# Kernel tuning notes

Measured on AMD Instinct MI355X. Metric: run time of the kernel, lower is better.

The kernel has to match this reference:

```python
import jax, jax.numpy as jnp
import numpy as np

N, E, T = 4096, 49152, 262144
H, EMB, AIN, EB, TB = 256, 64, 92, 80, 40
NBLK = 12  # 4 alignn * 2 EGGC + 4 gcn


def _ln(x, s, b):
    mu = jnp.mean(x, -1, keepdims=True)
    v = jnp.mean((x - mu) ** 2, -1, keepdims=True)
    return (x - mu) * jax.lax.rsqrt(v + 1e-5) * s + b


def _mlp(x, W, b, s, bi):
    # Linear -> LayerNorm -> SiLU (MLPLayer)
    return jax.nn.silu(_ln(x @ W + b, s, bi))


def _rbf(x, vmin, vmax, bins):
    centers = jnp.linspace(vmin, vmax, bins)
    gamma = 1.0 / ((vmax - vmin) / (bins - 1))
    return jnp.exp(-gamma * (x[:, None] - centers) ** 2)


def _eggc(x, e, src, dst, W, b, ln_s, ln_b, n_nodes):
    # W: [5,H,H] = src_gate, dst_gate, edge_gate, src_update, dst_update
    m = (x @ W[0] + b[0])[src] + (x @ W[1] + b[1])[dst] + (e @ W[2] + b[2])
    sigma = jax.nn.sigmoid(m)
    sum_sh = jax.ops.segment_sum((x @ W[4] + b[4])[src] * sigma, dst, num_segments=n_nodes)
    sum_s = jax.ops.segment_sum(sigma, dst, num_segments=n_nodes)
    h = sum_sh / (sum_s + 1e-6)
    x_new = jax.nn.silu(_ln(x @ W[3] + b[3] + h, ln_s[0], ln_b[0]))
    e_new = jax.nn.silu(_ln(m, ln_s[1], ln_b[1]))
    return x + x_new, e + e_new  # residual=True


def setup_inputs() -> dict:
    key = jax.random.key(0)
    ks = jax.random.split(key, 16)
    s = 0.05
    return {
        "atom_features": jax.random.normal(ks[0], (N, AIN), jnp.float32),
        "r": jax.random.normal(ks[1], (E, 3), jnp.float32),
        "src": jax.random.randint(ks[2], (E,), 0, N),
        "dst": jax.random.randint(ks[3], (E,), 0, N),
        "lsrc": jax.random.randint(ks[4], (T,), 0, E),
        "ldst": jax.random.randint(ks[5], (T,), 0, E),
        "atom_W": s * jax.random.normal(ks[6], (AIN, H), jnp.float32),
        "atom_b": jnp.zeros((H,), jnp.float32),
        "atom_ln_s": jnp.ones((H,), jnp.float32),
        "atom_ln_b": jnp.zeros((H,), jnp.float32),
        "edge_W1": s * jax.random.normal(ks[7], (EB, EMB), jnp.float32),
        "edge_b1": jnp.zeros((EMB,), jnp.float32),
        "edge_ln1_s": jnp.ones((EMB,), jnp.float32),
        "edge_ln1_b": jnp.zeros((EMB,), jnp.float32),
        "edge_W2": s * jax.random.normal(ks[8], (EMB, H), jnp.float32),
        "edge_b2": jnp.zeros((H,), jnp.float32),
        "edge_ln2_s": jnp.ones((H,), jnp.float32),
        "edge_ln2_b": jnp.zeros((H,), jnp.float32),
        "ang_W1": s * jax.random.normal(ks[9], (TB, EMB), jnp.float32),
        "ang_b1": jnp.zeros((EMB,), jnp.float32),
        "ang_ln1_s": jnp.ones((EMB,), jnp.float32),
        "ang_ln1_b": jnp.zeros((EMB,), jnp.float32),
        "ang_W2": s * jax.random.normal(ks[10], (EMB, H), jnp.float32),
        "ang_b2": jnp.zeros((H,), jnp.float32),
        "ang_ln2_s": jnp.ones((H,), jnp.float32),
        "ang_ln2_b": jnp.zeros((H,), jnp.float32),
        "eggc_W": s * jax.random.normal(ks[11], (NBLK, 5, H, H), jnp.float32),
        "eggc_b": jnp.zeros((NBLK, 5, H), jnp.float32),
        "eggc_ln_s": jnp.ones((NBLK, 2, H), jnp.float32),
        "eggc_ln_b": jnp.zeros((NBLK, 2, H), jnp.float32),
        "fc_W": s * jax.random.normal(ks[12], (H, 1), jnp.float32),
        "fc_b": jnp.zeros((1,), jnp.float32),
    }


def reference(atom_features, r, src, dst, lsrc, ldst,
              atom_W, atom_b, atom_ln_s, atom_ln_b,
              edge_W1, edge_b1, edge_ln1_s, edge_ln1_b,
              edge_W2, edge_b2, edge_ln2_s, edge_ln2_b,
              ang_W1, ang_b1, ang_ln1_s, ang_ln1_b,
              ang_W2, ang_b2, ang_ln2_s, ang_ln2_b,
              eggc_W, eggc_b, eggc_ln_s, eggc_ln_b, fc_W, fc_b):
    # line-graph bond cosines: cos(-r_i, r_j) for each bond pair
    r1, r2 = -r[lsrc], r[ldst]
    cos = jnp.sum(r1 * r2, -1) / (jnp.linalg.norm(r1, axis=-1) * jnp.linalg.norm(r2, axis=-1))
    cos = jnp.clip(cos, -1.0, 1.0)
    z = _mlp(_mlp(_rbf(cos, -1.0, 1.0, TB), ang_W1, ang_b1, ang_ln1_s, ang_ln1_b),
             ang_W2, ang_b2, ang_ln2_s, ang_ln2_b)
    x = _mlp(atom_features, atom_W, atom_b, atom_ln_s, atom_ln_b)
    bondlength = jnp.linalg.norm(r, axis=1)
    y = _mlp(_mlp(_rbf(bondlength, 0.0, 8.0, EB), edge_W1, edge_b1, edge_ln1_s, edge_ln1_b),
             edge_W2, edge_b2, edge_ln2_s, edge_ln2_b)
    for i in range(4):  # alignn layers: crystal graph then line graph
        x, m = _eggc(x, y, src, dst, eggc_W[2 * i], eggc_b[2 * i], eggc_ln_s[2 * i], eggc_ln_b[2 * i], N)
        y, z = _eggc(m, z, lsrc, ldst, eggc_W[2 * i + 1], eggc_b[2 * i + 1], eggc_ln_s[2 * i + 1], eggc_ln_b[2 * i + 1], E)
    for i in range(4):  # gcn layers
        j = 8 + i
        x, y = _eggc(x, y, src, dst, eggc_W[j], eggc_b[j], eggc_ln_s[j], eggc_ln_b[j], N)
    atomwise_energy = x @ fc_W + fc_b  # [N,1]
    total_energy = jnp.mean(atomwise_energy)  # AvgPooling (eV/atom), single graph
    return total_energy, atomwise_energy
```

## Files before the change

### kernel.cpp

```cpp
#include <hip/hip_runtime.h>


typedef unsigned short bfu;
typedef __attribute__((ext_vector_type(8))) short short8;
typedef __attribute__((ext_vector_type(4))) float floatx4;

#define CHN 4096
#define CHCAP 24576
#define HH 65536

__device__ __forceinline__ float bf2f(bfu u) {
  union { unsigned u; float f; } x; x.u = ((unsigned)u) << 16; return x.f;
}
__device__ __forceinline__ bfu f2bf(float f) {
  union { float f; unsigned u; } x; x.f = f;
  unsigned r = x.u + 0x7FFFu + ((x.u >> 16) & 1u);
  return (bfu)(r >> 16);
}
__device__ __forceinline__ float fsig(float x) {
  return __builtin_amdgcn_rcpf(1.f + __expf(-x));
}
__device__ __forceinline__ float fsilu(float x) { return x * fsig(x); }

struct f4 { float x, y, z, w; };
__device__ __forceinline__ f4 ld4(const bfu* p) {
  ushort4 u = *(const ushort4*)(const void*)p;
  return {bf2f(u.x), bf2f(u.y), bf2f(u.z), bf2f(u.w)};
}
__device__ __forceinline__ void st4(bfu* p, f4 v) {
  ushort4 u = {f2bf(v.x), f2bf(v.y), f2bf(v.z), f2bf(v.w)};
  *(ushort4*)(void*)p = u;
}
__device__ __forceinline__ f4 f4add(f4 a, f4 b) { return {a.x+b.x, a.y+b.y, a.z+b.z, a.w+b.w}; }
__device__ __forceinline__ f4 sig4(f4 m) {
  return {fsig(m.x), fsig(m.y), fsig(m.z), fsig(m.w)};
}
__device__ __forceinline__ void wstats(f4 v, float& mean, float& rstd) {
  float s = v.x+v.y+v.z+v.w;
  float q = v.x*v.x+v.y*v.y+v.z*v.z+v.w*v.w;
#pragma unroll
  for (int m = 1; m < 64; m <<= 1) { s += __shfl_xor(s, m); q += __shfl_xor(q, m); }
  mean = s * (1.f/256.f);
  rstd = rsqrtf(fmaxf(q*(1.f/256.f) - mean*mean, 0.f) + 1e-5f);
}
__device__ __forceinline__ f4 lnsilu4(f4 pre, f4 sg, f4 bb) {
  float mean, rstd; wstats(pre, mean, rstd);
  f4 u = {(pre.x-mean)*rstd*sg.x+bb.x, (pre.y-mean)*rstd*sg.y+bb.y,
          (pre.z-mean)*rstd*sg.z+bb.z, (pre.w-mean)*rstd*sg.w+bb.w};
  return {fsilu(u.x), fsilu(u.y), fsilu(u.z), fsilu(u.w)};
}
__device__ __forceinline__ float block_sum256(float t, float* sm) {
#pragma unroll
  for (int o = 32; o; o >>= 1) t += __shfl_down(t, o);
  if ((threadIdx.x & 63) == 0) sm[threadIdx.x >> 6] = t;
  __syncthreads();
  float r = sm[0] + sm[1] + sm[2] + sm[3];
  __syncthreads();
  return r;
}

__global__ void probe_kernel(const unsigned* __restrict__ ones_raw, int* __restrict__ mode) {
  if (threadIdx.x == 0) *mode = (ones_raw[0] == 0x3F800000u) ? 1 : 0;
}
__global__ __launch_bounds__(256) void cvt_kernel(
    const void* __restrict__ src, bfu* __restrict__ dst, int n, const int* __restrict__ mode) {
  int i = blockIdx.x * 256 + threadIdx.x;
  if (i >= n) return;
  dst[i] = (*mode) ? f2bf(((const float*)src)[i]) : ((const bfu*)src)[i];
}
__global__ __launch_bounds__(256) void cvtf_kernel(
    const void* __restrict__ src, float* __restrict__ dst, int n, const int* __restrict__ mode) {
  int i = blockIdx.x * 256 + threadIdx.x;
  if (i >= n) return;
  dst[i] = (*mode) ? ((const float*)src)[i] : bf2f(((const bfu*)src)[i]);
}
struct CvtDesc { const void* src; bfu* dst; int n; };
struct CvtPack { CvtDesc e[20]; };
__global__ __launch_bounds__(256) void cvt_batch_kernel(CvtPack p, const int* __restrict__ mode) {
  CvtDesc d = p.e[blockIdx.y];
  int i = blockIdx.x * 256 + threadIdx.x;
  if (i >= d.n) return;
  d.dst[i] = (*mode) ? f2bf(((const float*)d.src)[i]) : ((const bfu*)d.src)[i];
}

template<int BM, int BN, int WR, int WC>
__device__ __forceinline__ void gemm_body(
    const bfu* __restrict__ A, const bfu* __restrict__ Bt,
    const bfu* __restrict__ bias, bfu* __restrict__ Cout,
    int cnt, int N, int K, int base, int m0, int n0)
{
  constexpr int WM = BM / WR, WN = BN / WC;
  constexpr int TM = WM / 16, TN = WN / 16;
  constexpr int LDT = 72;
  static __shared__ bfu As[BM * LDT];
  static __shared__ bfu Bs[BN * LDT];

  const int tid = threadIdx.x, wave = tid >> 6, lane = tid & 63;
  const int wr = wave / WC, wc = wave % WC;
  const int lrow = lane & 15, kq = (lane >> 4) * 8;

  floatx4 acc[TM][TN];
#pragma unroll
  for (int i = 0; i < TM; ++i)
#pragma unroll
    for (int j = 0; j < TN; ++j) acc[i][j] = (floatx4){0.f, 0.f, 0.f, 0.f};

  constexpr int ACH = BM * 8, BCH = BN * 8;
  for (int k0 = 0; k0 < K; k0 += 64) {
#pragma unroll
    for (int idx = tid; idx < ACH; idx += 256) {
      int row = idx >> 3, kc = (idx & 7) << 3;
      int r = m0 + row;
      int ar = base + (r < cnt ? r : cnt - 1);
      *(short8*)(void*)(As + row * LDT + kc) =
          *(const short8*)(const void*)(A + (size_t)ar * K + k0 + kc);
    }
#pragma unroll
    for (int idx = tid; idx < BCH; idx += 256) {
      int row = idx >> 3, kc = (idx & 7) << 3;
      *(short8*)(void*)(Bs + row * LDT + kc) =
          *(const short8*)(const void*)(Bt + (size_t)(n0 + row) * K + k0 + kc);
    }
    __syncthreads();
#pragma unroll
    for (int s = 0; s < 2; ++s) {
      short8 Af[TM], Bf[TN];
#pragma unroll
      for (int i = 0; i < TM; ++i)
        Af[i] = *(const short8*)(const void*)(As + (wr * WM + i * 16 + lrow) * LDT + s * 32 + kq);
#pragma unroll
      for (int j = 0; j < TN; ++j)
        Bf[j] = *(const short8*)(const void*)(Bs + (wc * WN + j * 16 + lrow) * LDT + s * 32 + kq);
#pragma unroll
      for (int i = 0; i < TM; ++i)
#pragma unroll
        for (int j = 0; j < TN; ++j)
          acc[i][j] = __builtin_amdgcn_mfma_f32_16x16x32_bf16(Af[i], Bf[j], acc[i][j], 0, 0, 0);
    }
    __syncthreads();
  }

  const int rquad = lane >> 4, cin = lane & 15;
#pragma unroll
  for (int i = 0; i < TM; ++i) {
#pragma unroll
    for (int rr = 0; rr < 4; ++rr) {
      int orow = m0 + wr * WM + i * 16 + rquad * 4 + rr;
      if (orow >= cnt) continue;
#pragma unroll
      for (int j = 0; j < TN; ++j) {
        int gcol = n0 + wc * WN + j * 16 + cin;
        Cout[(size_t)orow * N + gcol] = f2bf(acc[i][j][rr] + bf2f(bias[gcol]));
      }
    }
  }
}

template<int BM, int BN, int WR, int WC>
__global__ __launch_bounds__(256) void gemm_kernel(
    const bfu* __restrict__ A, const bfu* __restrict__ Bt,
    const bfu* __restrict__ bias, bfu* __restrict__ Cout, int M, int N, int K)
{
  gemm_body<BM, BN, WR, WC>(A, Bt, bias, Cout, M, N, K, 0,
                            blockIdx.x * BM, blockIdx.y * BN);
}

__global__ __launch_bounds__(256) void line_gemm_kernel(
    const bfu* __restrict__ z, const bfu* __restrict__ yb,
    const bfu* __restrict__ W, const bfu* __restrict__ bb,
    bfu* __restrict__ mchunk, bfu* __restrict__ u3c,
    const int* __restrict__ loff, int n0, int n1)
{
  if (blockIdx.y < 2) {
    int base = loff[n0], cnt = loff[n1] - base;
    int m0 = blockIdx.x * 128;
    if (m0 >= cnt) return;
    gemm_body<128, 128, 2, 2>(z, W + 4 * HH, bb + 4 * 256, mchunk,
                              cnt, 256, 256, base, m0, blockIdx.y * 128);
  } else {
    if (blockIdx.x >= 64) return;
    gemm_body<128, 128, 2, 2>(yb + (size_t)n0 * 256, W + 3 * HH, bb + 3 * 256, u3c,
                              CHN, 256, 256, 0, (blockIdx.x & 31) * 128, (blockIdx.x >> 5) * 128);
  }
}

__global__ __launch_bounds__(256) void cosbl_kernel(
    const float* __restrict__ r, const int* __restrict__ lsrc_p,
    const int* __restrict__ ldst_p, float* __restrict__ cosv,
    float* __restrict__ bl, int T, int E)
{
  int idx = blockIdx.x * 256 + threadIdx.x;
  if (idx < T) {
    int e1 = lsrc_p[idx], e2 = ldst_p[idx];
    float ax = -r[e1 * 3 + 0], ay = -r[e1 * 3 + 1], az = -r[e1 * 3 + 2];
    float bx =  r[e2 * 3 + 0], by =  r[e2 * 3 + 1], bz =  r[e2 * 3 + 2];
    float dot = ax * bx + ay * by + az * bz;
    float na = sqrtf(ax * ax + ay * ay + az * az);
    float nb = sqrtf(bx * bx + by * by + bz * bz);
    float c = dot / (na * nb);
    cosv[idx] = fminf(1.f, fmaxf(-1.f, c));
  } else if (idx < T + E) {
    int e = idx - T;
    float x = r[e * 3 + 0], yv = r[e * 3 + 1], zv = r[e * 3 + 2];
    bl[e] = sqrtf(x * x + yv * yv + zv * zv);
  }
}

template<int KP, int BINS, int IS_ANG>
__global__ __launch_bounds__(256) void mlp1_ln_kernel(
    const float* __restrict__ v, const bfu* __restrict__ Bt,
    const bfu* __restrict__ bias, const bfu* __restrict__ lns,
    const bfu* __restrict__ lnb, bfu* __restrict__ outp, int M)
{
  constexpr int LDT = KP + 8;
  __shared__ bfu As[128 * LDT];
  __shared__ bfu Bs[64 * LDT];
  const int tid = threadIdx.x, wave = tid >> 6, lane = tid & 63;
  const int lrow = lane & 15, kq = (lane >> 4) * 8;
  const int m0 = blockIdx.x * 128;

  for (int idx = tid; idx < 128 * (KP / 8); idx += 256) {
    int row = idx / (KP / 8), kc = (idx % (KP / 8)) * 8;
    float val = v[m0 + row];
    short8 pack;
#pragma unroll
    for (int jj = 0; jj < 8; ++jj) {
      int k = kc + jj;
      float e = 0.f;
      if (k < BINS) {
        float center = IS_ANG ? (-1.f + k * (2.f / 39.f)) : (k * (8.f / 79.f));
        float d = val - center;
        e = __expf((IS_ANG ? -19.5f : -9.875f) * d * d);
      }
      ((bfu*)&pack)[jj] = f2bf(e);
    }
    *(short8*)(void*)(As + row * LDT + kc) = pack;
  }
  for (int idx = tid; idx < 64 * (KP / 8); idx += 256) {
    int row = idx / (KP / 8), kc = (idx % (KP / 8)) * 8;
    *(short8*)(void*)(Bs + row * LDT + kc) =
        *(const short8*)(const void*)(Bt + (size_t)row * KP + kc);
  }
  __syncthreads();

  floatx4 acc[2][4];
#pragma unroll
  for (int i = 0; i < 2; ++i)
#pragma unroll
    for (int j = 0; j < 4; ++j) acc[i][j] = (floatx4){0.f, 0.f, 0.f, 0.f};
#pragma unroll
  for (int ks = 0; ks < KP / 32; ++ks) {
    short8 Af[2], Bf[4];
#pragma unroll
    for (int i = 0; i < 2; ++i)
      Af[i] = *(const short8*)(const void*)(As + (wave * 32 + i * 16 + lrow) * LDT + ks * 32 + kq);
#pragma unroll
    for (int j = 0; j < 4; ++j)
      Bf[j] = *(const short8*)(const void*)(Bs + (j * 16 + lrow) * LDT + ks * 32 + kq);
#pragma unroll
    for (int i = 0; i < 2; ++i)
#pragma unroll
      for (int j = 0; j < 4; ++j)
        acc[i][j] = __builtin_amdgcn_mfma_f32_16x16x32_bf16(Af[i], Bf[j], acc[i][j], 0, 0, 0);
  }

  const int rquad = lane >> 4, cin = lane & 15;
  float bj[4], sj[4], lj[4];
#pragma unroll
  for (int j = 0; j < 4; ++j) {
    bj[j] = bf2f(bias[j * 16 + cin]);
    sj[j] = bf2f(lns[j * 16 + cin]);
    lj[j] = bf2f(lnb[j * 16 + cin]);
  }
#pragma unroll
  for (int i = 0; i < 2; ++i) {
#pragma unroll
    for (int rr = 0; rr < 4; ++rr) {
      int row = m0 + wave * 32 + i * 16 + rquad * 4 + rr;
      float pre[4], s = 0.f, q = 0.f;
#pragma unroll
      for (int j = 0; j < 4; ++j) {
        pre[j] = acc[i][j][rr] + bj[j];
        s += pre[j]; q += pre[j] * pre[j];
      }
#pragma unroll
      for (int mm = 1; mm < 16; mm <<= 1) { s += __shfl_xor(s, mm); q += __shfl_xor(q, mm); }
      float mean = s * (1.f / 64.f);
      float rstd = rsqrtf(fmaxf(q * (1.f / 64.f) - mean * mean, 0.f) + 1e-5f);
#pragma unroll
      for (int j = 0; j < 4; ++j) {
        float u = (pre[j] - mean) * rstd * sj[j] + lj[j];
        outp[(size_t)row * 64 + j * 16 + cin] = f2bf(fsilu(u));
      }
    }
  }
}

__global__ __launch_bounds__(256) void mlp2_ln_kernel(
    const bfu* __restrict__ A, const bfu* __restrict__ Bt,
    const bfu* __restrict__ bias, const bfu* __restrict__ lns,
    const bfu* __restrict__ lnb, bfu* __restrict__ outp, int M)
{
  __shared__ bfu As[64 * 72];
  __shared__ bfu Bs[256 * 72];
  __shared__ float part[64 * 8];
  const int tid = threadIdx.x, wave = tid >> 6, lane = tid & 63;
  const int lrow = lane & 15, kq = (lane >> 4) * 8;
  const int m0 = blockIdx.x * 64;

  for (int idx = tid; idx < 512; idx += 256) {
    int row = idx >> 3, kc = (idx & 7) << 3;
    *(short8*)(void*)(As + row * 72 + kc) =
        *(const short8*)(const void*)(A + (size_t)(m0 + row) * 64 + kc);
  }
  for (int idx = tid; idx < 2048; idx += 256) {
    int row = idx >> 3, kc = (idx & 7) << 3;
    *(short8*)(void*)(Bs + row * 72 + kc) =
        *(const short8*)(const void*)(Bt + (size_t)row * 64 + kc);
  }
  __syncthreads();

  floatx4 acc[4][4];
#pragma unroll
  for (int i = 0; i < 4; ++i)
#pragma unroll
    for (int j = 0; j < 4; ++j) acc[i][j] = (floatx4){0.f, 0.f, 0.f, 0.f};
#pragma unroll
  for (int s = 0; s < 2; ++s) {
    short8 Af[4], Bf[4];
#pragma unroll
    for (int i = 0; i < 4; ++i)
      Af[i] = *(const short8*)(const void*)(As + (i * 16 + lrow) * 72 + s * 32 + kq);
#pragma unroll
    for (int j = 0; j < 4; ++j)
      Bf[j] = *(const short8*)(const void*)(Bs + (wave * 64 + j * 16 + lrow) * 72 + s * 32 + kq);
#pragma unroll
    for (int i = 0; i < 4; ++i)
#pragma unroll
      for (int j = 0; j < 4; ++j)
        acc[i][j] = __builtin_amdgcn_mfma_f32_16x16x32_bf16(Af[i], Bf[j], acc[i][j], 0, 0, 0);
  }

  const int rquad = lane >> 4, cin = lane & 15;
  float bj[4], sj[4], lj[4];
#pragma unroll
  for (int j = 0; j < 4; ++j) {
    int col = wave * 64 + j * 16 + cin;
    bj[j] = bf2f(bias[col]); sj[j] = bf2f(lns[col]); lj[j] = bf2f(lnb[col]);
  }
#pragma unroll
  for (int i = 0; i < 4; ++i) {
#pragma unroll
    for (int rr = 0; rr < 4; ++rr) {
      float s = 0.f, q = 0.f;
#pragma unroll
      for (int j = 0; j < 4; ++j) {
        float p = acc[i][j][rr] + bj[j];
        s += p; q += p * p;
      }
#pragma unroll
      for (int mm = 1; mm < 16; mm <<= 1) { s += __shfl_xor(s, mm); q += __shfl_xor(q, mm); }
      if (cin == 0) {
        int row = i * 16 + rquad * 4 + rr;
        part[row * 8 + wave * 2] = s;
        part[row * 8 + wave * 2 + 1] = q;
      }
    }
  }
  __syncthreads();
#pragma unroll
  for (int i = 0; i < 4; ++i) {
#pragma unroll
    for (int rr = 0; rr < 4; ++rr) {
      int row = i * 16 + rquad * 4 + rr;
      float s = part[row * 8] + part[row * 8 + 2] + part[row * 8 + 4] + part[row * 8 + 6];
      float q = part[row * 8 + 1] + part[row * 8 + 3] + part[row * 8 + 5] + part[row * 8 + 7];
      float mean = s * (1.f / 256.f);
      float rstd = rsqrtf(fmaxf(q * (1.f / 256.f) - mean * mean, 0.f) + 1e-5f);
#pragma unroll
      for (int j = 0; j < 4; ++j) {
        float u = (acc[i][j][rr] + bj[j] - mean) * rstd * sj[j] + lj[j];
        outp[(size_t)(m0 + row) * 256 + wave * 64 + j * 16 + cin] = f2bf(fsilu(u));
      }
    }
  }
}

__global__ __launch_bounds__(256) void count_kernel(
    const int* __restrict__ d, int* __restrict__ cnt, int ne) {
  int i = blockIdx.x * 256 + threadIdx.x;
  if (i < ne) atomicAdd(&cnt[d[i]], 1);
}
__global__ __launch_bounds__(256) void scan_kernel(
    const int* __restrict__ cnt, int* __restrict__ off, int n) {
  __shared__ int ssum[256];
  __shared__ int sbase[257];
  int t = threadIdx.x;
  int strip = (n + 255) / 256;
  int lo = t * strip, hi = lo + strip; if (hi > n) hi = n; if (lo > n) lo = n;
  int s = 0;
  for (int i = lo; i < hi; ++i) s += cnt[i];
  ssum[t] = s;
  __syncthreads();
  if (t == 0) {
    int run = 0;
    for (int i = 0; i < 256; ++i) { sbase[i] = run; run += ssum[i]; }
    sbase[256] = run;
  }
  __syncthreads();
  int run = sbase[t];
  for (int i = lo; i < hi; ++i) { off[i] = run; run += cnt[i]; }
  if (t == 0) off[n] = sbase[256];
}
__global__ __launch_bounds__(256) void copy_kernel(
    const int* __restrict__ a, int* __restrict__ b, int n) {
  int i = blockIdx.x * 256 + threadIdx.x;
  if (i < n) b[i] = a[i];
}
__global__ __launch_bounds__(256) void fill_kernel(
    const int* __restrict__ d, int* __restrict__ cur, int* __restrict__ ids, int ne) {
  int i = blockIdx.x * 256 + threadIdx.x;
  if (i < ne) ids[atomicAdd(&cur[d[i]], 1)] = i;
}
__global__ __launch_bounds__(256) void fill2_kernel(
    const int* __restrict__ ldst, const int* __restrict__ lsrc, int* __restrict__ cur,
    int* __restrict__ lsrc_p, int* __restrict__ ldst_p, int ne) {
  int i = blockIdx.x * 256 + threadIdx.x;
  if (i >= ne) return;
  int d = ldst[i];
  int pos = atomicAdd(&cur[d], 1);
  lsrc_p[pos] = lsrc[i];
  ldst_p[pos] = d;
}

__global__ __launch_bounds__(256) void transpose_pad_kernel(
    const void* __restrict__ W, bfu* __restrict__ Wt, int K, int N, int Kp,
    const int* __restrict__ mode)
{
  int idx = blockIdx.x * 256 + threadIdx.x;
  if (idx >= N * Kp) return;
  int n = idx / Kp, k = idx - n * Kp;
  bfu v = 0;
  if (k < K) {
    size_t si = (size_t)k * N + n;
    v = (*mode) ? f2bf(((const float*)W)[si]) : ((const bfu*)W)[si];
  }
  Wt[idx] = v;
}
__device__ __forceinline__ int slot2mat(int slot) {
  const int m[5] = {0, 4, 1, 3, 2};
  return m[slot];
}
__global__ __launch_bounds__(256) void transpose_eggc_kernel(
    const void* __restrict__ W, bfu* __restrict__ Wt, const int* __restrict__ mode)
{
  int bs = blockIdx.y;
  int blk = bs / 5, slot = bs - blk * 5;
  int mat = slot2mat(slot);
  int idx = blockIdx.x * 256 + threadIdx.x;
  int n = idx >> 8, k = idx & 255;
  size_t si = ((size_t)(blk * 5 + mat) * 256 + k) * 256 + n;
  bfu v = (*mode) ? f2bf(((const float*)W)[si]) : ((const bfu*)W)[si];
  Wt[((size_t)bs * 256 + n) * 256 + k] = v;
}
__global__ __launch_bounds__(256) void bias_perm_kernel(
    const void* __restrict__ B, bfu* __restrict__ Bp, const int* __restrict__ mode)
{
  int i = blockIdx.x * 256 + threadIdx.x;
  int bs = i >> 8, c = i & 255;
  int blk = bs / 5, slot = bs - blk * 5;
  int mat = slot2mat(slot);
  size_t si = (size_t)(blk * 5 + mat) * 256 + c;
  Bp[i] = (*mode) ? f2bf(((const float*)B)[si]) : ((const bfu*)B)[si];
}

__global__ __launch_bounds__(256) void atom_fused_kernel(
    const bfu* __restrict__ mbuf, const bfu* __restrict__ af,
    const int* __restrict__ src, const int* __restrict__ dst,
    bfu* __restrict__ X, bfu* __restrict__ Y,
    const int* __restrict__ aoff, const int* __restrict__ aids,
    int eblk,
    const bfu* __restrict__ lns, const bfu* __restrict__ lnb,
    const bfu* __restrict__ les, const bfu* __restrict__ leb)
{
  int wave = threadIdx.x >> 6, c4 = (threadIdx.x & 63) * 4;
  if ((int)blockIdx.x < eblk) {
    int e = blockIdx.x * 4 + wave;
    f4 m = f4add(f4add(ld4(mbuf + (size_t)e * 256 + c4),
                       ld4(af + (size_t)src[e] * 1024 + c4)),
                 ld4(af + (size_t)dst[e] * 1024 + 512 + c4));
    f4 sil = lnsilu4(m, ld4(les + c4), ld4(leb + c4));
    bfu* op = Y + (size_t)e * 256 + c4;
    st4(op, f4add(sil, ld4(op)));
  } else {
    int n = (blockIdx.x - eblk) * 4 + wave;
    int p0 = aoff[n], p1 = aoff[n + 1];
    f4 g1 = ld4(af + (size_t)n * 1024 + 512 + c4);
    f4 num = {0, 0, 0, 0}, den = {0, 0, 0, 0};
    for (int p = p0; p < p1; ++p) {
      int id = aids[p], sx = src[id];
      f4 m = f4add(f4add(ld4(mbuf + (size_t)id * 256 + c4),
                         ld4(af + (size_t)sx * 1024 + c4)), g1);
      f4 sg = sig4(m);
      f4 u4 = ld4(af + (size_t)sx * 1024 + 256 + c4);
      num.x += sg.x * u4.x; num.y += sg.y * u4.y; num.z += sg.z * u4.z; num.w += sg.w * u4.w;
      den = f4add(den, sg);
    }
    f4 u3 = ld4(af + (size_t)n * 1024 + 768 + c4);
    f4 pre = {u3.x + num.x / (den.x + 1e-6f), u3.y + num.y / (den.y + 1e-6f),
              u3.z + num.z / (den.z + 1e-6f), u3.w + num.w / (den.w + 1e-6f)};
    f4 sil = lnsilu4(pre, ld4(lns + c4), ld4(lnb + c4));
    bfu* op = X + (size_t)n * 256 + c4;
    st4(op, f4add(sil, ld4(op)));
  }
}

__global__ __launch_bounds__(256) void line_fused_kernel(
    const bfu* __restrict__ mchunk, const bfu* __restrict__ lf,
    const bfu* __restrict__ u3c,
    const int* __restrict__ loff, const int* __restrict__ lsrc_p,
    const int* __restrict__ ldst_p,
    bfu* __restrict__ Z, bfu* __restrict__ Y,
    int n0, int eblk,
    const bfu* __restrict__ lns, const bfu* __restrict__ lnb,
    const bfu* __restrict__ les, const bfu* __restrict__ leb)
{
  int wave = threadIdx.x >> 6, c4 = (threadIdx.x & 63) * 4;
  int base = loff[n0];
  if ((int)blockIdx.x < eblk) {
    int rloc = blockIdx.x * 4 + wave;
    int cnt = loff[n0 + CHN] - base;
    if (rloc >= cnt) return;
    int p = base + rloc;
    f4 m = f4add(f4add(ld4(mchunk + (size_t)rloc * 256 + c4),
                       ld4(lf + (size_t)lsrc_p[p] * 768 + c4)),
                 ld4(lf + (size_t)ldst_p[p] * 768 + 512 + c4));
    f4 sil = lnsilu4(m, ld4(les + c4), ld4(leb + c4));
    bfu* op = Z + (size_t)p * 256 + c4;
    st4(op, f4add(sil, ld4(op)));
  } else {
    int n = n0 + (blockIdx.x - eblk) * 4 + wave;
    int p0 = loff[n], p1 = loff[n + 1];
    f4 g1 = ld4(lf + (size_t)n * 768 + 512 + c4);
    f4 num = {0, 0, 0, 0}, den = {0, 0, 0, 0};
    for (int p = p0; p < p1; ++p) {
      int sx = lsrc_p[p];
      f4 m = f4add(f4add(ld4(mchunk + (size_t)(p - base) * 256 + c4),
                         ld4(lf + (size_t)sx * 768 + c4)), g1);
      f4 sg = sig4(m);
      f4 u4 = ld4(lf + (size_t)sx * 768 + 256 + c4);
      num.x += sg.x * u4.x; num.y += sg.y * u4.y; num.z += sg.z * u4.z; num.w += sg.w * u4.w;
      den = f4add(den, sg);
    }
    f4 u3 = ld4(u3c + (size_t)(n - n0) * 256 + c4);
    f4 pre = {u3.x + num.x / (den.x + 1e-6f), u3.y + num.y / (den.y + 1e-6f),
              u3.z + num.z / (den.z + 1e-6f), u3.w + num.w / (den.w + 1e-6f)};
    f4 sil = lnsilu4(pre, ld4(lns + c4), ld4(lnb + c4));
    bfu* op = Y + (size_t)n * 256 + c4;
    st4(op, f4add(sil, ld4(op)));
  }
}

__global__ __launch_bounds__(256) void atom_init_kernel(
    const bfu* __restrict__ af, const bfu* __restrict__ W, const bfu* __restrict__ bias,
    const bfu* __restrict__ lns, const bfu* __restrict__ lnb, bfu* __restrict__ X)
{
  __shared__ float sm[4];
  int row = blockIdx.x, c = threadIdx.x;
  float acc = bf2f(bias[c]);
  for (int k = 0; k < 92; ++k)
    acc += bf2f(af[row * 92 + k]) * bf2f(W[k * 256 + c]);
  float mean = block_sum256(acc, sm) * (1.f / 256.f);
  float d = acc - mean;
  float var = block_sum256(d * d, sm) * (1.f / 256.f);
  float u = d * rsqrtf(var + 1e-5f) * bf2f(lns[c]) + bf2f(lnb[c]);
  X[(size_t)row * 256 + c] = f2bf(fsilu(u));
}

__global__ __launch_bounds__(256) void final_kernel(
    const bfu* __restrict__ X, const bfu* __restrict__ fcW, const bfu* __restrict__ fcb,
    void* __restrict__ out, float* __restrict__ acc, const int* __restrict__ mode)
{
  int row = blockIdx.x * 4 + (threadIdx.x >> 6);
  int lane = threadIdx.x & 63;
  float s = 0.f;
#pragma unroll
  for (int k = 0; k < 4; ++k)
    s += bf2f(X[(size_t)row * 256 + lane + k * 64]) * bf2f(fcW[lane + k * 64]);
#pragma unroll
  for (int o = 32; o; o >>= 1) s += __shfl_down(s, o);
  if (lane == 0) {
    float v = s + bf2f(fcb[0]);
    if (*mode) ((float*)out)[1 + row] = v;
    else       ((bfu*)out)[1 + row] = f2bf(v);
    atomicAdd(acc, v);
  }
}
__global__ void mean_kernel(const float* __restrict__ acc, void* __restrict__ out,
                            const int* __restrict__ mode) {
  if (threadIdx.x == 0) {
    float v = acc[0] * (1.f / 4096.f);
    if (*mode) ((float*)out)[0] = v;
    else       ((bfu*)out)[0] = f2bf(v);
  }
}
__global__ void dbg_kernel(void* __restrict__ out, float v) {
  if (threadIdx.x == 0) { ((bfu*)out)[0] = f2bf(v); }
}

static void gemm128(const bfu* A, const bfu* Bt, const bfu* bias, bfu* C,
                    int M, int N, int K, hipStream_t st) {
  if (N % 128 == 0) {
    dim3 g(M / 128, N / 128);
    gemm_kernel<128, 128, 2, 2><<<g, 256, 0, st>>>(A, Bt, bias, C, M, N, K);
  } else {
    dim3 g(M / 128, N / 64);
    gemm_kernel<128, 64, 4, 1><<<g, 256, 0, st>>>(A, Bt, bias, C, M, N, K);
  }
}

extern "C" void kernel_launch(void* const* d_in, const int* in_sizes, int n_in,
                              void* d_out, int out_size, void* d_ws, size_t ws_size,
                              hipStream_t stream) {
  const int N = 4096, E = 49152, T = 262144, H = 256;

  const int* src  = (const int*)d_in[2];
  const int* dst  = (const int*)d_in[3];
  const int* lsrc = (const int*)d_in[4];
  const int* ldst = (const int*)d_in[5];

  char* bp = (char*)d_ws;
  size_t off = 0;
  auto carve = [&](size_t bytes) -> char* {
    char* q = bp + off;
    off = (off + bytes + 255) & ~(size_t)255;
    return q;
  };
  bfu* x       = (bfu*)carve((size_t)N * H * 2);
  bfu* y       = (bfu*)carve((size_t)E * H * 2);
  bfu* z       = (bfu*)carve((size_t)T * H * 2);
  bfu* reg     = (bfu*)carve((size_t)E * 768 * 2);
  bfu* u3c     = (bfu*)carve((size_t)CHN * H * 2);
  bfu* mchunk  = (bfu*)carve((size_t)CHCAP * H * 2);
  bfu* WtE     = (bfu*)carve((size_t)60 * H * H * 2);
  bfu* ebp     = (bfu*)carve((size_t)12 * 5 * H * 2);
  bfu* Wt_a1   = (bfu*)carve(64 * 64 * 2);
  bfu* Wt_a2   = (bfu*)carve(256 * 64 * 2);
  bfu* Wt_e1   = (bfu*)carve(64 * 128 * 2);
  bfu* Wt_e2   = (bfu*)carve(256 * 64 * 2);
  int* aoff    = (int*)carve((size_t)(N + 1) * 4);
  int* aids    = (int*)carve((size_t)E * 4);
  int* loff    = (int*)carve((size_t)(E + 1) * 4);
  int* lsrc_p  = (int*)carve((size_t)T * 4);
  int* ldst_p  = (int*)carve((size_t)T * 4);
  int* cursors = (int*)carve((size_t)E * 4);
  float* macc  = (float*)carve(256);
  int* mode    = (int*)carve(256);
  bfu* par_c   = (bfu*)carve(8192 * 2);
  bfu* els_c   = (bfu*)carve((size_t)12 * 2 * H * 2);
  bfu* elb_c   = (bfu*)carve((size_t)12 * 2 * H * 2);

  if (off > ws_size) {
    hipMemsetAsync(d_out, 0, (size_t)out_size * 2, stream);
    dbg_kernel<<<1, 64, 0, stream>>>(d_out, (float)(ws_size >> 20));
    return;
  }

  char* tail = (char*)reg + (size_t)52 * 1024 * 1024;
  bfu* af_c  = (bfu*)tail;                 tail += ((size_t)N * 92 * 2 + 255) & ~255ull;
  float* r_f = (float*)tail;               tail += ((size_t)E * 3 * 4 + 255) & ~255ull;
  float* cosv = (float*)tail;              tail += ((size_t)T * 4 + 255) & ~255ull;
  float* blv = (float*)tail;               tail += ((size_t)E * 4 + 255) & ~255ull;
  bfu* atW_c = (bfu*)tail;

  bfu* atom_b_c   = par_c + 0;
  bfu* atom_lns_c = par_c + 256;
  bfu* atom_lnb_c = par_c + 512;
  bfu* e_b1_c     = par_c + 768;
  bfu* e_l1s_c    = par_c + 832;
  bfu* e_l1b_c    = par_c + 896;
  bfu* e_b2_c     = par_c + 1024;
  bfu* e_l2s_c    = par_c + 1280;
  bfu* e_l2b_c    = par_c + 1536;
  bfu* a_b1_c     = par_c + 1792;
  bfu* a_l1s_c    = par_c + 1856;
  bfu* a_l1b_c    = par_c + 1920;
  bfu* a_b2_c     = par_c + 2048;
  bfu* a_l2s_c    = par_c + 2304;
  bfu* a_l2b_c    = par_c + 2560;
  bfu* fcW_c      = par_c + 2816;
  bfu* fcb_c      = par_c + 3072;

  bfu* lfused = reg;
  bfu* afused = reg;
  bfu* mbufa  = reg + (size_t)N * 1024;
  bfu* emb_t  = reg;
  bfu* emb_e  = reg + (size_t)T * 64;

  probe_kernel<<<1, 64, 0, stream>>>((const unsigned*)d_in[8], mode);
  CvtPack pk;
  int ii = 0;
  auto add = [&](int idx, bfu* dstp, int n) { pk.e[ii++] = {d_in[idx], dstp, n}; };
  add(7, atom_b_c, 256);  add(8, atom_lns_c, 256); add(9, atom_lnb_c, 256);
  add(11, e_b1_c, 64);    add(12, e_l1s_c, 64);    add(13, e_l1b_c, 64);
  add(15, e_b2_c, 256);   add(16, e_l2s_c, 256);   add(17, e_l2b_c, 256);
  add(19, a_b1_c, 64);    add(20, a_l1s_c, 64);    add(21, a_l1b_c, 64);
  add(23, a_b2_c, 256);   add(24, a_l2s_c, 256);   add(25, a_l2b_c, 256);
  add(30, fcW_c, 256);    add(31, fcb_c, 1);
  add(28, els_c, 12 * 2 * 256);
  add(29, elb_c, 12 * 2 * 256);
  add(6, atW_c, 92 * 256);
  cvt_batch_kernel<<<dim3(92, 20), 256, 0, stream>>>(pk, mode);
  cvt_kernel<<<(N * 92 + 255) / 256, 256, 0, stream>>>(d_in[0], af_c, N * 92, mode);
  cvtf_kernel<<<(E * 3 + 255) / 256, 256, 0, stream>>>(d_in[1], r_f, E * 3, mode);

  hipMemsetAsync(cursors, 0, (size_t)N * 4, stream);
  count_kernel<<<E / 256, 256, 0, stream>>>(dst, cursors, E);
  scan_kernel<<<1, 256, 0, stream>>>(cursors, aoff, N);
  copy_kernel<<<(N + 255) / 256, 256, 0, stream>>>(aoff, cursors, N);
  fill_kernel<<<E / 256, 256, 0, stream>>>(dst, cursors, aids, E);

  hipMemsetAsync(cursors, 0, (size_t)E * 4, stream);
  count_kernel<<<T / 256, 256, 0, stream>>>(ldst, cursors, T);
  scan_kernel<<<1, 256, 0, stream>>>(cursors, loff, E);
  copy_kernel<<<(E + 255) / 256, 256, 0, stream>>>(loff, cursors, E);
  fill2_kernel<<<T / 256, 256, 0, stream>>>(ldst, lsrc, cursors, lsrc_p, ldst_p, T);

  transpose_eggc_kernel<<<dim3(256, 60), 256, 0, stream>>>(d_in[26], WtE, mode);
  bias_perm_kernel<<<60, 256, 0, stream>>>(d_in[27], ebp, mode);
  transpose_pad_kernel<<<16, 256, 0, stream>>>(d_in[18], Wt_a1, 40, 64, 64, mode);
  transpose_pad_kernel<<<64, 256, 0, stream>>>(d_in[22], Wt_a2, 64, 256, 64, mode);
  transpose_pad_kernel<<<32, 256, 0, stream>>>(d_in[10], Wt_e1, 80, 64, 128, mode);
  transpose_pad_kernel<<<64, 256, 0, stream>>>(d_in[14], Wt_e2, 64, 256, 64, mode);

  cosbl_kernel<<<(T + E + 255) / 256, 256, 0, stream>>>(r_f, lsrc_p, ldst_p, cosv, blv, T, E);
  mlp1_ln_kernel<64, 40, 1><<<T / 128, 256, 0, stream>>>(
      cosv, Wt_a1, a_b1_c, a_l1s_c, a_l1b_c, emb_t, T);
  mlp2_ln_kernel<<<T / 64, 256, 0, stream>>>(emb_t, Wt_a2, a_b2_c, a_l2s_c, a_l2b_c, z, T);
  mlp1_ln_kernel<128, 80, 0><<<E / 128, 256, 0, stream>>>(
      blv, Wt_e1, e_b1_c, e_l1s_c, e_l1b_c, emb_e, E);
  mlp2_ln_kernel<<<E / 64, 256, 0, stream>>>(emb_e, Wt_e2, e_b2_c, e_l2s_c, e_l2b_c, y, E);

  atom_init_kernel<<<N, 256, 0, stream>>>(af_c, atW_c, atom_b_c, atom_lns_c, atom_lnb_c, x);

  auto atom_eggc = [&](int blk, int do_edge) {
    const bfu* W  = WtE + (size_t)blk * 5 * HH;
    const bfu* bb = ebp + (size_t)blk * 5 * H;
    const bfu* ls = els_c + (size_t)blk * 2 * H;
    const bfu* lb = elb_c + (size_t)blk * 2 * H;
    gemm128(x, W, bb, afused, N, 1024, H, stream);
    gemm128(y, W + 4 * HH, bb + 4 * H, mbufa, E, H, H, stream);
    int eblk = do_edge ? E / 4 : 0;
    atom_fused_kernel<<<eblk + N / 4, 256, 0, stream>>>(
        mbufa, afused, src, dst, x, y, aoff, aids, eblk, ls, lb, ls + H, lb + H);
  };

  auto line_eggc = [&](int blk, int do_edge) {
    const bfu* W  = WtE + (size_t)blk * 5 * HH;
    const bfu* bb = ebp + (size_t)blk * 5 * H;
    const bfu* ls = els_c + (size_t)blk * 2 * H;
    const bfu* lb = elb_c + (size_t)blk * 2 * H;
    gemm128(y, W, bb, lfused, E, 768, H, stream);
    for (int c = 0; c < E / CHN; ++c) {
      int n0 = c * CHN;
      line_gemm_kernel<<<dim3(CHCAP / 128, 3), 256, 0, stream>>>(
          z, y, W, bb, mchunk, u3c, loff, n0, n0 + CHN);
      int eblk = do_edge ? CHCAP / 4 : 0;
      line_fused_kernel<<<eblk + CHN / 4, 256, 0, stream>>>(
          mchunk, lfused, u3c, loff, lsrc_p, ldst_p, z, y, n0, eblk,
          ls, lb, ls + H, lb + H);
    }
  };

  for (int i = 0; i < 4; ++i) {
    atom_eggc(2 * i, 1);
    line_eggc(2 * i + 1, i < 3);
  }
  for (int i = 0; i < 4; ++i)
    atom_eggc(8 + i, i < 3);

  hipMemsetAsync(macc, 0, 4, stream);
  final_kernel<<<N / 4, 256, 0, stream>>>(x, fcW_c, fcb_c, d_out, macc, mode);
  mean_kernel<<<1, 64, 0, stream>>>(macc, d_out, mode);
}
```

Before: 3.012 ms.

## Merge EGGC gemm launches, widen fused kernels to 8-wide, load MLP weights directly

The two atom-side GEMMs become one launch, and the line-graph gate GEMM is merged with the first chunk's edge/u3 GEMMs. The fused edge and node kernels now use 8-element vector loads with half-wave rows, so each wave handles two edges, or splits a node's neighbour loop across two halves and combines them with a shuffle. The MLP kernels read weight fragments straight from global memory instead of staging them in LDS. The goal is fewer launches, wider memory transactions and more memory-level parallelism in the gathers. The risks are lower occupancy from extra registers and uncoalesced global weight reads.

```diff
diff --git a/kernel.cpp b/kernel.cpp
--- a/kernel.cpp
+++ b/kernel.cpp
@@ -22,33 +22,50 @@
 }
 __device__ __forceinline__ float fsilu(float x) { return x * fsig(x); }
 
-struct f4 { float x, y, z, w; };
-__device__ __forceinline__ f4 ld4(const bfu* p) {
-  ushort4 u = *(const ushort4*)(const void*)p;
-  return {bf2f(u.x), bf2f(u.y), bf2f(u.z), bf2f(u.w)};
-}
-__device__ __forceinline__ void st4(bfu* p, f4 v) {
-  ushort4 u = {f2bf(v.x), f2bf(v.y), f2bf(v.z), f2bf(v.w)};
-  *(ushort4*)(void*)p = u;
-}
-__device__ __forceinline__ f4 f4add(f4 a, f4 b) { return {a.x+b.x, a.y+b.y, a.z+b.z, a.w+b.w}; }
-__device__ __forceinline__ f4 sig4(f4 m) {
-  return {fsig(m.x), fsig(m.y), fsig(m.z), fsig(m.w)};
-}
-__device__ __forceinline__ void wstats(f4 v, float& mean, float& rstd) {
-  float s = v.x+v.y+v.z+v.w;
-  float q = v.x*v.x+v.y*v.y+v.z*v.z+v.w*v.w;
-#pragma unroll
-  for (int m = 1; m < 64; m <<= 1) { s += __shfl_xor(s, m); q += __shfl_xor(q, m); }
-  mean = s * (1.f/256.f);
-  rstd = rsqrtf(fmaxf(q*(1.f/256.f) - mean*mean, 0.f) + 1e-5f);
-}
-__device__ __forceinline__ f4 lnsilu4(f4 pre, f4 sg, f4 bb) {
-  float mean, rstd; wstats(pre, mean, rstd);
-  f4 u = {(pre.x-mean)*rstd*sg.x+bb.x, (pre.y-mean)*rstd*sg.y+bb.y,
-          (pre.z-mean)*rstd*sg.z+bb.z, (pre.w-mean)*rstd*sg.w+bb.w};
-  return {fsilu(u.x), fsilu(u.y), fsilu(u.z), fsilu(u.w)};
-}
+struct f8 { float v[8]; };
+__device__ __forceinline__ f8 ld8(const bfu* p) {
+  short8 u = *(const short8*)(const void*)p;
+  f8 r;
+#pragma unroll
+  for (int i = 0; i < 8; ++i) r.v[i] = bf2f((bfu)u[i]);
+  return r;
+}
+__device__ __forceinline__ void st8(bfu* p, f8 x) {
+  short8 u;
+#pragma unroll
+  for (int i = 0; i < 8; ++i) u[i] = (short)f2bf(x.v[i]);
+  *(short8*)(void*)p = u;
+}
+__device__ __forceinline__ f8 add8(f8 a, f8 b) {
+  f8 r;
+#pragma unroll
+  for (int i = 0; i < 8; ++i) r.v[i] = a.v[i] + b.v[i];
+  return r;
+}
+__device__ __forceinline__ f8 sig8(f8 m) {
+  f8 r;
+#pragma unroll
+  for (int i = 0; i < 8; ++i) r.v[i] = fsig(m.v[i]);
+  return r;
+}
+__device__ __forceinline__ void wstats32(const f8& x, float& mean, float& rstd) {
+  float s = 0.f, q = 0.f;
+#pragma unroll
+  for (int i = 0; i < 8; ++i) { s += x.v[i]; q += x.v[i] * x.v[i]; }
+#pragma unroll
+  for (int m = 1; m < 32; m <<= 1) { s += __shfl_xor(s, m); q += __shfl_xor(q, m); }
+  mean = s * (1.f / 256.f);
+  rstd = rsqrtf(fmaxf(q * (1.f / 256.f) - mean * mean, 0.f) + 1e-5f);
+}
+__device__ __forceinline__ f8 lnsilu8(f8 pre, f8 sg, f8 bb) {
+  float mean, rstd; wstats32(pre, mean, rstd);
+  f8 r;
+#pragma unroll
+  for (int i = 0; i < 8; ++i)
+    r.v[i] = fsilu((pre.v[i] - mean) * rstd * sg.v[i] + bb.v[i]);
+  return r;
+}
+
 __device__ __forceinline__ float block_sum256(float t, float* sm) {
 #pragma unroll
   for (int o = 32; o; o >>= 1) t += __shfl_down(t, o);
@@ -180,6 +197,43 @@
   } else {
     if (blockIdx.x >= 64) return;
     gemm_body<128, 128, 2, 2>(yb + (size_t)n0 * 256, W + 3 * HH, bb + 3 * 256, u3c,
+                              CHN, 256, 256, 0, (blockIdx.x & 31) * 128, (blockIdx.x >> 5) * 128);
+  }
+}
+
+__global__ __launch_bounds__(256) void atom_gemm_kernel(
+    const bfu* __restrict__ x, const bfu* __restrict__ y,
+    const bfu* __restrict__ W, const bfu* __restrict__ bb,
+    bfu* __restrict__ afused, bfu* __restrict__ mbufa)
+{
+  if (blockIdx.x < 384) {
+    gemm_body<128, 128, 2, 2>(y, W + 4 * HH, bb + 4 * 256, mbufa,
+                              49152, 256, 256, 0, blockIdx.x * 128, blockIdx.y * 128);
+  } else {
+    int lid = (blockIdx.x - 384) * 2 + blockIdx.y;
+    gemm_body<128, 128, 2, 2>(x, W, bb, afused,
+                              4096, 1024, 256, 0, (lid >> 3) * 128, (lid & 7) * 128);
+  }
+}
+
+__global__ __launch_bounds__(256) void line_gates_kernel(
+    const bfu* __restrict__ y, const bfu* __restrict__ z,
+    const bfu* __restrict__ W, const bfu* __restrict__ bb,
+    bfu* __restrict__ lfused, bfu* __restrict__ mchunk, bfu* __restrict__ u3c,
+    const int* __restrict__ loff)
+{
+  if (blockIdx.y < 6) {
+    gemm_body<128, 128, 2, 2>(y, W, bb, lfused,
+                              49152, 768, 256, 0, blockIdx.x * 128, blockIdx.y * 128);
+  } else if (blockIdx.y < 8) {
+    int cnt = loff[CHN];
+    int m0 = blockIdx.x * 128;
+    if (blockIdx.x >= CHCAP / 128 || m0 >= cnt) return;
+    gemm_body<128, 128, 2, 2>(z, W + 4 * HH, bb + 4 * 256, mchunk,
+                              cnt, 256, 256, 0, m0, (blockIdx.y - 6) * 128);
+  } else {
+    if (blockIdx.x >= 64) return;
+    gemm_body<128, 128, 2, 2>(y, W + 3 * HH, bb + 3 * 256, u3c,
                               CHN, 256, 256, 0, (blockIdx.x & 31) * 128, (blockIdx.x >> 5) * 128);
   }
 }
@@ -214,7 +268,6 @@
 {
   constexpr int LDT = KP + 8;
   __shared__ bfu As[128 * LDT];
-  __shared__ bfu Bs[64 * LDT];
   const int tid = threadIdx.x, wave = tid >> 6, lane = tid & 63;
   const int lrow = lane & 15, kq = (lane >> 4) * 8;
   const int m0 = blockIdx.x * 128;
@@ -232,14 +285,9 @@
         float d = val - center;
         e = __expf((IS_ANG ? -19.5f : -9.875f) * d * d);
       }
-      ((bfu*)&pack)[jj] = f2bf(e);
+      pack[jj] = (short)f2bf(e);
     }
     *(short8*)(void*)(As + row * LDT + kc) = pack;
-  }
-  for (int idx = tid; idx < 64 * (KP / 8); idx += 256) {
-    int row = idx / (KP / 8), kc = (idx % (KP / 8)) * 8;
-    *(short8*)(void*)(Bs + row * LDT + kc) =
-        *(const short8*)(const void*)(Bt + (size_t)row * KP + kc);
   }
   __syncthreads();
 
@@ -252,11 +300,11 @@
   for (int ks = 0; ks < KP / 32; ++ks) {
     short8 Af[2], Bf[4];
 #pragma unroll
+    for (int j = 0; j < 4; ++j)
+      Bf[j] = *(const short8*)(const void*)(Bt + (size_t)(j * 16 + lrow) * KP + ks * 32 + kq);
+#pragma unroll
     for (int i = 0; i < 2; ++i)
       Af[i] = *(const short8*)(const void*)(As + (wave * 32 + i * 16 + lrow) * LDT + ks * 32 + kq);
-#pragma unroll
-    for (int j = 0; j < 4; ++j)
-      Bf[j] = *(const short8*)(const void*)(Bs + (j * 16 + lrow) * LDT + ks * 32 + kq);
 #pragma unroll
     for (int i = 0; i < 2; ++i)
 #pragma unroll
@@ -302,22 +350,24 @@
     const bfu* __restrict__ lnb, bfu* __restrict__ outp, int M)
 {
   __shared__ bfu As[64 * 72];
-  __shared__ bfu Bs[256 * 72];
   __shared__ float part[64 * 8];
   const int tid = threadIdx.x, wave = tid >> 6, lane = tid & 63;
   const int lrow = lane & 15, kq = (lane >> 4) * 8;
   const int m0 = blockIdx.x * 64;
 
+  short8 Bf[2][4];
+#pragma unroll
+  for (int s = 0; s < 2; ++s)
+#pragma unroll
+    for (int j = 0; j < 4; ++j)
+      Bf[s][j] = *(const short8*)(const void*)(
+          Bt + (size_t)(wave * 64 + j * 16 + lrow) * 64 + s * 32 + kq);
+
   for (int idx = tid; idx < 512; idx += 256) {
     int row = idx >> 3, kc = (idx & 7) << 3;
     *(short8*)(void*)(As + row * 72 + kc) =
         *(const short8*)(const void*)(A + (size_t)(m0 + row) * 64 + kc);
   }
-  for (int idx = tid; idx < 2048; idx += 256) {
-    int row = idx >> 3, kc = (idx & 7) << 3;
-    *(short8*)(void*)(Bs + row * 72 + kc) =
-        *(const short8*)(const void*)(Bt + (size_t)row * 64 + kc);
-  }
   __syncthreads();
 
   floatx4 acc[4][4];
@@ -327,18 +377,15 @@
     for (int j = 0; j < 4; ++j) acc[i][j] = (floatx4){0.f, 0.f, 0.f, 0.f};
 #pragma unroll
   for (int s = 0; s < 2; ++s) {
-    short8 Af[4], Bf[4];
+    short8 Af[4];
 #pragma unroll
     for (int i = 0; i < 4; ++i)
       Af[i] = *(const short8*)(const void*)(As + (i * 16 + lrow) * 72 + s * 32 + kq);
 #pragma unroll
-    for (int j = 0; j < 4; ++j)
-      Bf[j] = *(const short8*)(const void*)(Bs + (wave * 64 + j * 16 + lrow) * 72 + s * 32 + kq);
-#pragma unroll
     for (int i = 0; i < 4; ++i)
 #pragma unroll
       for (int j = 0; j < 4; ++j)
-        acc[i][j] = __builtin_amdgcn_mfma_f32_16x16x32_bf16(Af[i], Bf[j], acc[i][j], 0, 0, 0);
+        acc[i][j] = __builtin_amdgcn_mfma_f32_16x16x32_bf16(Af[i], Bf[s][j], acc[i][j], 0, 0, 0);
   }
 
   const int rquad = lane >> 4, cin = lane & 15;
@@ -483,35 +530,48 @@
     const bfu* __restrict__ lns, const bfu* __restrict__ lnb,
     const bfu* __restrict__ les, const bfu* __restrict__ leb)
 {
-  int wave = threadIdx.x >> 6, c4 = (threadIdx.x & 63) * 4;
+  int wave = threadIdx.x >> 6, lane = threadIdx.x & 63;
+  int half = lane >> 5, c8 = (lane & 31) * 8;
   if ((int)blockIdx.x < eblk) {
-    int e = blockIdx.x * 4 + wave;
-    f4 m = f4add(f4add(ld4(mbuf + (size_t)e * 256 + c4),
-                       ld4(af + (size_t)src[e] * 1024 + c4)),
-                 ld4(af + (size_t)dst[e] * 1024 + 512 + c4));
-    f4 sil = lnsilu4(m, ld4(les + c4), ld4(leb + c4));
-    bfu* op = Y + (size_t)e * 256 + c4;
-    st4(op, f4add(sil, ld4(op)));
+    int e = blockIdx.x * 8 + wave * 2 + half;
+    f8 m = add8(add8(ld8(mbuf + (size_t)e * 256 + c8),
+                     ld8(af + (size_t)src[e] * 1024 + c8)),
+                ld8(af + (size_t)dst[e] * 1024 + 512 + c8));
+    f8 sil = lnsilu8(m, ld8(les + c8), ld8(leb + c8));
+    bfu* op = Y + (size_t)e * 256 + c8;
+    st8(op, add8(sil, ld8(op)));
   } else {
     int n = (blockIdx.x - eblk) * 4 + wave;
     int p0 = aoff[n], p1 = aoff[n + 1];
-    f4 g1 = ld4(af + (size_t)n * 1024 + 512 + c4);
-    f4 num = {0, 0, 0, 0}, den = {0, 0, 0, 0};
-    for (int p = p0; p < p1; ++p) {
+    f8 g1 = ld8(af + (size_t)n * 1024 + 512 + c8);
+    f8 num = {}, den = {};
+    for (int p = p0 + half; p < p1; p += 2) {
       int id = aids[p], sx = src[id];
-      f4 m = f4add(f4add(ld4(mbuf + (size_t)id * 256 + c4),
-                         ld4(af + (size_t)sx * 1024 + c4)), g1);
-      f4 sg = sig4(m);
-      f4 u4 = ld4(af + (size_t)sx * 1024 + 256 + c4);
-      num.x += sg.x * u4.x; num.y += sg.y * u4.y; num.z += sg.z * u4.z; num.w += sg.w * u4.w;
-      den = f4add(den, sg);
-    }
-    f4 u3 = ld4(af + (size_t)n * 1024 + 768 + c4);
-    f4 pre = {u3.x + num.x / (den.x + 1e-6f), u3.y + num.y / (den.y + 1e-6f),
-              u3.z + num.z / (den.z + 1e-6f), u3.w + num.w / (den.w + 1e-6f)};
-    f4 sil = lnsilu4(pre, ld4(lns + c4), ld4(lnb + c4));
-    bfu* op = X + (size_t)n * 256 + c4;
-    st4(op, f4add(sil, ld4(op)));
+      f8 m = add8(add8(ld8(mbuf + (size_t)id * 256 + c8),
+                       ld8(af + (size_t)sx * 1024 + c8)), g1);
+      f8 sg = sig8(m);
+      f8 u4 = ld8(af + (size_t)sx * 1024 + 256 + c8);
+#pragma unroll
+      for (int i = 0; i < 8; ++i) {
+        num.v[i] += sg.v[i] * u4.v[i];
+        den.v[i] += sg.v[i];
+      }
+    }
+#pragma unroll
+    for (int i = 0; i < 8; ++i) {
+      num.v[i] += __shfl_xor(num.v[i], 32);
+      den.v[i] += __shfl_xor(den.v[i], 32);
+    }
+    f8 u3 = ld8(af + (size_t)n * 1024 + 768 + c8);
+    f8 pre;
+#pragma unroll
+    for (int i = 0; i < 8; ++i)
+      pre.v[i] = u3.v[i] + num.v[i] / (den.v[i] + 1e-6f);
+    f8 sil = lnsilu8(pre, ld8(lns + c8), ld8(lnb + c8));
+    if (half == 0) {
+      bfu* op = X + (size_t)n * 256 + c8;
+      st8(op, add8(sil, ld8(op)));
+    }
   }
 }
 
@@ -525,39 +585,52 @@
     const bfu* __restrict__ lns, const bfu* __restrict__ lnb,
     const bfu* __restrict__ les, const bfu* __restrict__ leb)
 {
-  int wave = threadIdx.x >> 6, c4 = (threadIdx.x & 63) * 4;
+  int wave = threadIdx.x >> 6, lane = threadIdx.x & 63;
+  int half = lane >> 5, c8 = (lane & 31) * 8;
   int base = loff[n0];
   if ((int)blockIdx.x < eblk) {
-    int rloc = blockIdx.x * 4 + wave;
+    int rloc = blockIdx.x * 8 + wave * 2 + half;
     int cnt = loff[n0 + CHN] - base;
     if (rloc >= cnt) return;
     int p = base + rloc;
-    f4 m = f4add(f4add(ld4(mchunk + (size_t)rloc * 256 + c4),
-                       ld4(lf + (size_t)lsrc_p[p] * 768 + c4)),
-                 ld4(lf + (size_t)ldst_p[p] * 768 + 512 + c4));
-    f4 sil = lnsilu4(m, ld4(les + c4), ld4(leb + c4));
-    bfu* op = Z + (size_t)p * 256 + c4;
-    st4(op, f4add(sil, ld4(op)));
+    f8 m = add8(add8(ld8(mchunk + (size_t)rloc * 256 + c8),
+                     ld8(lf + (size_t)lsrc_p[p] * 768 + c8)),
+                ld8(lf + (size_t)ldst_p[p] * 768 + 512 + c8));
+    f8 sil = lnsilu8(m, ld8(les + c8), ld8(leb + c8));
+    bfu* op = Z + (size_t)p * 256 + c8;
+    st8(op, add8(sil, ld8(op)));
   } else {
     int n = n0 + (blockIdx.x - eblk) * 4 + wave;
     int p0 = loff[n], p1 = loff[n + 1];
-    f4 g1 = ld4(lf + (size_t)n * 768 + 512 + c4);
-    f4 num = {0, 0, 0, 0}, den = {0, 0, 0, 0};
-    for (int p = p0; p < p1; ++p) {
+    f8 g1 = ld8(lf + (size_t)n * 768 + 512 + c8);
+    f8 num = {}, den = {};
+    for (int p = p0 + half; p < p1; p += 2) {
       int sx = lsrc_p[p];
-      f4 m = f4add(f4add(ld4(mchunk + (size_t)(p - base) * 256 + c4),
-                         ld4(lf + (size_t)sx * 768 + c4)), g1);
-      f4 sg = sig4(m);
-      f4 u4 = ld4(lf + (size_t)sx * 768 + 256 + c4);
-      num.x += sg.x * u4.x; num.y += sg.y * u4.y; num.z += sg.z * u4.z; num.w += sg.w * u4.w;
-      den = f4add(den, sg);
-    }
-    f4 u3 = ld4(u3c + (size_t)(n - n0) * 256 + c4);
-    f4 pre = {u3.x + num.x / (den.x + 1e-6f), u3.y + num.y / (den.y + 1e-6f),
-              u3.z + num.z / (den.z + 1e-6f), u3.w + num.w / (den.w + 1e-6f)};
-    f4 sil = lnsilu4(pre, ld4(lns + c4), ld4(lnb + c4));
-    bfu* op = Y + (size_t)n * 256 + c4;
-    st4(op, f4add(sil, ld4(op)));
+      f8 m = add8(add8(ld8(mchunk + (size_t)(p - base) * 256 + c8),
+                       ld8(lf + (size_t)sx * 768 + c8)), g1);
+      f8 sg = sig8(m);
+      f8 u4 = ld8(lf + (size_t)sx * 768 + 256 + c8);
+#pragma unroll
+      for (int i = 0; i < 8; ++i) {
+        num.v[i] += sg.v[i] * u4.v[i];
+        den.v[i] += sg.v[i];
+      }
+    }
+#pragma unroll
+    for (int i = 0; i < 8; ++i) {
+      num.v[i] += __shfl_xor(num.v[i], 32);
+      den.v[i] += __shfl_xor(den.v[i], 32);
+    }
+    f8 u3 = ld8(u3c + (size_t)(n - n0) * 256 + c8);
+    f8 pre;
+#pragma unroll
+    for (int i = 0; i < 8; ++i)
+      pre.v[i] = u3.v[i] + num.v[i] / (den.v[i] + 1e-6f);
+    f8 sil = lnsilu8(pre, ld8(lns + c8), ld8(lnb + c8));
+    if (half == 0) {
+      bfu* op = Y + (size_t)n * 256 + c8;
+      st8(op, add8(sil, ld8(op)));
+    }
   }
 }
 
@@ -610,13 +683,8 @@
 
 static void gemm128(const bfu* A, const bfu* Bt, const bfu* bias, bfu* C,
                     int M, int N, int K, hipStream_t st) {
-  if (N % 128 == 0) {
-    dim3 g(M / 128, N / 128);
-    gemm_kernel<128, 128, 2, 2><<<g, 256, 0, st>>>(A, Bt, bias, C, M, N, K);
-  } else {
-    dim3 g(M / 128, N / 64);
-    gemm_kernel<128, 64, 4, 1><<<g, 256, 0, st>>>(A, Bt, bias, C, M, N, K);
-  }
+  dim3 g(M / 128, N / 128);
+  gemm_kernel<128, 128, 2, 2><<<g, 256, 0, st>>>(A, Bt, bias, C, M, N, K);
 }
 
 extern "C" void kernel_launch(void* const* d_in, const int* in_sizes, int n_in,
@@ -748,9 +816,8 @@
     const bfu* bb = ebp + (size_t)blk * 5 * H;
     const bfu* ls = els_c + (size_t)blk * 2 * H;
     const bfu* lb = elb_c + (size_t)blk * 2 * H;
-    gemm128(x, W, bb, afused, N, 1024, H, stream);
-    gemm128(y, W + 4 * HH, bb + 4 * H, mbufa, E, H, H, stream);
-    int eblk = do_edge ? E / 4 : 0;
+    atom_gemm_kernel<<<dim3(512, 2), 256, 0, stream>>>(x, y, W, bb, afused, mbufa);
+    int eblk = do_edge ? E / 8 : 0;
     atom_fused_kernel<<<eblk + N / 4, 256, 0, stream>>>(
         mbufa, afused, src, dst, x, y, aoff, aids, eblk, ls, lb, ls + H, lb + H);
   };
@@ -760,15 +827,17 @@
     const bfu* bb = ebp + (size_t)blk * 5 * H;
     const bfu* ls = els_c + (size_t)blk * 2 * H;
     const bfu* lb = elb_c + (size_t)blk * 2 * H;
-    gemm128(y, W, bb, lfused, E, 768, H, stream);
+    line_gates_kernel<<<dim3(384, 9), 256, 0, stream>>>(
+        y, z, W, bb, lfused, mchunk, u3c, loff);
     for (int c = 0; c < E / CHN; ++c) {
       int n0 = c * CHN;
-      line_gemm_kernel<<<dim3(CHCAP / 128, 3), 256, 0, stream>>>(
-          z, y, W, bb, mchunk, u3c, loff, n0, n0 + CHN);
-      int eblk = do_edge ? CHCAP / 4 : 0;
+      int eblk = do_edge ? CHCAP / 8 : 0;
       line_fused_kernel<<<eblk + CHN / 4, 256, 0, stream>>>(
           mchunk, lfused, u3c, loff, lsrc_p, ldst_p, z, y, n0, eblk,
           ls, lb, ls + H, lb + H);
+      if (c + 1 < E / CHN)
+        line_gemm_kernel<<<dim3(CHCAP / 128, 3), 256, 0, stream>>>(
+            z, y, W, bb, mchunk, u3c, loff, n0 + CHN, n0 + 2 * CHN);
     }
   };
 
```

Result: faster. 2.870 ms (-4.7%).
